# Kernel optimization log

Hardware: AMD Instinct MI355X
Metric: run time of the kernel (lower is better)

Reference implementation:

```python
import jax, jax.numpy as jnp
import numpy as np

S, B, C = 7, 2, 20          # YOLOv1 grid / boxes / classes
NE = B * 5 + C              # 30 channels per cell
BATCH = 32768
NBOX = 4                    # ground-truth boxes per image
L_COORD = 5.0


def _encode_np(boxes, classes):
    """Vectorized numpy replica of YoloLoss.encode, including its quirks:
    conf written at channel 4 + S*k (=> 4 and 11), class at channel 10 which is
    then overwritten by wh_y*S via the s+2:s+4 slice for k=1 (s=7 -> 9:11).
    boxes: [N, nb, 4] in xyxy, classes: [N, nb] int."""
    N, nb = classes.shape
    t = np.zeros((N, S, S, NE), np.float32)
    wh = boxes[:, :, 2:] - boxes[:, :, :2]
    cxcy = (boxes[:, :, 2:] + boxes[:, :, :2]) / 2.0
    cell = 1.0 / S
    ij = np.ceil(cxcy / cell) - 1.0                 # [N, nb, 2] (col, row)
    ijc = np.clip(ij, 0, S - 1).astype(np.int64)
    img = np.repeat(np.arange(N), nb)
    col = ijc[:, :, 0].ravel()
    row = ijc[:, :, 1].ravel()
    whf = (wh * S).reshape(-1, 2).astype(np.float32)
    delta = ((cxcy - ij * cell) / cell).reshape(-1, 2).astype(np.float32)
    cls = classes.ravel().astype(np.float32)
    t[img, row, col, 4] = 1.0          # conf, k=0 (4 + S*0)
    t[img, row, col, 11] = 1.0         # conf, k=1 (4 + S*1)
    t[img, row, col, 10] = cls         # class id (will be clobbered below)
    t[img, row, col, 2:4] = whf        # k=0 wh
    t[img, row, col, 0:2] = delta      # k=0 xy
    t[img, row, col, 9:11] = whf       # k=1 wh -- overwrites channel 10!
    t[img, row, col, 7:9] = delta      # k=1 xy
    return t.reshape(N, S * S, NE)


def setup_inputs() -> dict:
    key = jax.random.key(0)
    prediction = jax.random.normal(key, (BATCH, S * S, NE), dtype=jnp.float32)
    rng = np.random.default_rng(0)
    cxcy = rng.uniform(0.15, 0.85, (BATCH, NBOX, 2)).astype(np.float32)
    wh = rng.uniform(0.05, 0.3, (BATCH, NBOX, 2)).astype(np.float32)
    boxes = np.concatenate([cxcy - wh / 2, cxcy + wh / 2], axis=-1)  # xyxy
    classes = rng.integers(0, C, (BATCH, NBOX))
    target = jnp.asarray(_encode_np(boxes, classes))
    return {"prediction": prediction, "target": target}


def _point_form(b):
    # cxcywh -> xyxy on last axis
    return jnp.concatenate([b[..., :2] - b[..., 2:4] / 2,
                            b[..., :2] + b[..., 2:4] / 2], axis=-1)


def _iou(a, b):
    # a: [..., Bp, 4], b: [..., Bt, 4] (xyxy) -> [..., Bp, Bt]
    a = a[..., :, None, :]
    b = b[..., None, :, :]
    lo = jnp.maximum(a[..., :2], b[..., :2])
    hi = jnp.minimum(a[..., 2:], b[..., 2:])
    inter = jnp.prod(jnp.clip(hi - lo, 0.0, None), axis=-1)
    area_a = jnp.prod(a[..., 2:] - a[..., :2], axis=-1)
    area_b = jnp.prod(b[..., 2:] - b[..., :2], axis=-1)
    return inter / (area_a + area_b - inter + 1e-12)


def reference(prediction, target):
    coord = target[:, :, 4] > 0                         # [N, G] cells with objects
    bp = prediction[:, :, :B * 5].reshape(*prediction.shape[:2], B, 5)
    bt = target[:, :, :B * 5].reshape(*target.shape[:2], B, 5)

    # responsible-box matching: iou[bp_i, bt_j], argmax over predicted boxes per target box
    iou = _iou(_point_form(bp[..., :4]), _point_form(bt[..., :4]))  # [N,G,Bp,Bt]
    idx = jnp.argmax(iou, axis=-2)                                  # [N,G,Bt]
    resp = (jax.nn.one_hot(idx, B, dtype=jnp.float32).sum(-2) > 0)  # dedup, [N,G,B]
    resp = resp & coord[..., None]
    resp_f = resp.astype(jnp.float32)
    cnt = jnp.maximum(resp_f.sum(), 1.0)

    # containment loss: BCE-with-logits, mean over responsible boxes
    conf_p = bp[..., 4]
    conf_t = bt[..., 4]
    bce = jnp.logaddexp(0.0, conf_p) - conf_p * conf_t
    contain_loss = jnp.sum(bce * resp_f) / cnt

    # localization loss: mean MSE on xy + mean MSE on wh over responsible boxes
    sq_xy = (bp[..., 0:2] - bt[..., 0:2]) ** 2
    sq_wh = (bp[..., 2:4] - bt[..., 2:4]) ** 2
    loc_loss = (jnp.sum(sq_xy * resp_f[..., None]) / (2.0 * cnt)
                + jnp.sum(sq_wh * resp_f[..., None]) / (2.0 * cnt))

    # class loss: cross-entropy, mean over object cells
    logits = prediction[:, :, B * 5:]                               # [N,G,C]
    cls = jnp.clip(jnp.floor(target[:, :, B * 5]), 0, C - 1).astype(jnp.int32)
    lsm = jax.nn.log_softmax(logits, axis=-1)
    nll = -jnp.take_along_axis(lsm, cls[..., None], axis=-1)[..., 0]
    coord_f = coord.astype(jnp.float32)
    class_loss = jnp.sum(nll * coord_f) / jnp.maximum(coord_f.sum(), 1.0)

    # NOTE: original also computes l_noobj * noobj MSE into total_loss but then
    # returns class + contain + l_coord*loc, so noobj is dead code.
    return class_loss + contain_loss + L_COORD * loc_loss
```

## Files before the change

kernel.cpp:

```cpp
#include <hip/hip_runtime.h>
#include <math.h>

#define NCELL (32768 * 49)
#define NE 30
#define NC 20
#define G1 2048
#define BLK 256
#define TTOT (G1 * BLK)


__device__ __forceinline__ void process_cell(
    const float* __restrict__ pred, const float* __restrict__ targ, int cell,
    float& a0, float& a1, float& a2, float& a3, float& a4, float& a5) {

    const float2* p2 = reinterpret_cast<const float2*>(pred + (size_t)cell * NE);
    const float2* t2 = reinterpret_cast<const float2*>(targ + (size_t)cell * NE);

    float p[30], t[12];
    #pragma unroll
    for (int i = 0; i < 15; ++i) { float2 v = p2[i]; p[2*i] = v.x; p[2*i+1] = v.y; }
    #pragma unroll
    for (int i = 0; i < 6; ++i)  { float2 v = t2[i]; t[2*i] = v.x; t[2*i+1] = v.y; }

    float iou[2][2];
    #pragma unroll
    for (int i = 0; i < 2; ++i) {
        const float pcx = p[5*i], pcy = p[5*i+1], pw = p[5*i+2], ph = p[5*i+3];
        const float alx = pcx - pw*0.5f, aly = pcy - ph*0.5f;
        const float ahx = pcx + pw*0.5f, ahy = pcy + ph*0.5f;
        const float area_a = pw * ph;
        #pragma unroll
        for (int j = 0; j < 2; ++j) {
            const float tcx = t[5*j], tcy = t[5*j+1], tw = t[5*j+2], th = t[5*j+3];
            const float blx = tcx - tw*0.5f, bly = tcy - th*0.5f;
            const float bhx = tcx + tw*0.5f, bhy = tcy + th*0.5f;
            float ix = fminf(ahx, bhx) - fmaxf(alx, blx);
            float iy = fminf(ahy, bhy) - fmaxf(aly, bly);
            ix = fmaxf(ix, 0.f); iy = fmaxf(iy, 0.f);
            const float inter = ix * iy;
            const float area_b = tw * th;
            iou[i][j] = inter / (area_a + area_b - inter + 1e-12f);
        }
    }
    const int idx0 = (iou[1][0] > iou[0][0]) ? 1 : 0;
    const int idx1 = (iou[1][1] > iou[0][1]) ? 1 : 0;

    #pragma unroll
    for (int k = 0; k < 2; ++k) {
        const bool resp = (idx0 == k || idx1 == k);
        if (resp) {
            a0 += 1.f;
            const float cp = p[5*k+4], ct = t[5*k+4];
            a1 += fmaxf(cp, 0.f) + log1pf(expf(-fabsf(cp))) - cp * ct;
            const float dx = p[5*k]   - t[5*k];
            const float dy = p[5*k+1] - t[5*k+1];
            a2 += dx*dx + dy*dy;
            const float dw = p[5*k+2] - t[5*k+2];
            const float dh = p[5*k+3] - t[5*k+3];
            a3 += dw*dw + dh*dh;
        }
    }

    a5 += 1.f;
    const float cf = fminf(fmaxf(floorf(t[10]), 0.f), 19.f);
    const int cls = (int)cf;
    float m = p[10];
    #pragma unroll
    for (int c = 1; c < NC; ++c) m = fmaxf(m, p[10 + c]);
    float se = 0.f;
    float sel = 0.f;
    #pragma unroll
    for (int c = 0; c < NC; ++c) {
        se += expf(p[10 + c] - m);
        sel += (c == cls) ? p[10 + c] : 0.f;
    }
    a4 += -(sel - m - logf(se));
}

__global__ __launch_bounds__(BLK) void yolo_partial(
    const float* __restrict__ pred,
    const float* __restrict__ targ,
    float* __restrict__ partial) {

    float a0 = 0.f, a1 = 0.f, a2 = 0.f, a3 = 0.f, a4 = 0.f, a5 = 0.f;

    const int tid = blockIdx.x * BLK + threadIdx.x;

    float t4v[4];
    t4v[0] = targ[(size_t)(tid)            * NE + 4];
    t4v[1] = targ[(size_t)(tid + TTOT)     * NE + 4];
    t4v[2] = targ[(size_t)(tid + 2 * TTOT) * NE + 4];
    t4v[3] = (tid + 3 * TTOT < NCELL) ? targ[(size_t)(tid + 3 * TTOT) * NE + 4] : 0.f;

    if (t4v[0] > 0.f) process_cell(pred, targ, tid,            a0, a1, a2, a3, a4, a5);
    if (t4v[1] > 0.f) process_cell(pred, targ, tid + TTOT,     a0, a1, a2, a3, a4, a5);
    if (t4v[2] > 0.f) process_cell(pred, targ, tid + 2 * TTOT, a0, a1, a2, a3, a4, a5);
    if (t4v[3] > 0.f) process_cell(pred, targ, tid + 3 * TTOT, a0, a1, a2, a3, a4, a5);

    #pragma unroll
    for (int off = 32; off > 0; off >>= 1) {
        a0 += __shfl_down(a0, off, 64);
        a1 += __shfl_down(a1, off, 64);
        a2 += __shfl_down(a2, off, 64);
        a3 += __shfl_down(a3, off, 64);
        a4 += __shfl_down(a4, off, 64);
        a5 += __shfl_down(a5, off, 64);
    }

    __shared__ float sm[4][6];
    const int wave = threadIdx.x >> 6;
    const int lane = threadIdx.x & 63;
    if (lane == 0) {
        sm[wave][0] = a0; sm[wave][1] = a1; sm[wave][2] = a2;
        sm[wave][3] = a3; sm[wave][4] = a4; sm[wave][5] = a5;
    }
    __syncthreads();
    if (threadIdx.x == 0) {
        #pragma unroll
        for (int k = 0; k < 6; ++k) {
            float s = sm[0][k] + sm[1][k] + sm[2][k] + sm[3][k];
            partial[blockIdx.x * 6 + k] = s;
        }
    }
}

__global__ __launch_bounds__(BLK) void yolo_final(
    const float* __restrict__ partial, float* __restrict__ out) {
    __shared__ double sm[BLK][6];
    double a[6] = {0, 0, 0, 0, 0, 0};
    for (int i = threadIdx.x; i < G1; i += BLK) {
        #pragma unroll
        for (int k = 0; k < 6; ++k) a[k] += (double)partial[i * 6 + k];
    }
    #pragma unroll
    for (int k = 0; k < 6; ++k) sm[threadIdx.x][k] = a[k];
    __syncthreads();
    for (int off = BLK / 2; off > 0; off >>= 1) {
        if (threadIdx.x < off) {
            #pragma unroll
            for (int k = 0; k < 6; ++k) sm[threadIdx.x][k] += sm[threadIdx.x + off][k];
        }
        __syncthreads();
    }
    if (threadIdx.x == 0) {
        const double resp_sum  = sm[0][0];
        const double bce_sum   = sm[0][1];
        const double sqxy_sum  = sm[0][2];
        const double sqwh_sum  = sm[0][3];
        const double nll_sum   = sm[0][4];
        const double coord_sum = sm[0][5];
        const double cnt = fmax(resp_sum, 1.0);
        const double contain_loss = bce_sum / cnt;
        const double loc_loss = (sqxy_sum + sqwh_sum) / (2.0 * cnt);
        const double class_loss = nll_sum / fmax(coord_sum, 1.0);
        out[0] = (float)(class_loss + contain_loss + 5.0 * loc_loss);
    }
}

extern "C" void kernel_launch(void* const* d_in, const int* in_sizes, int n_in,
                              void* d_out, int out_size, void* d_ws, size_t ws_size,
                              hipStream_t stream) {
    const float* pred = (const float*)d_in[0];
    const float* targ = (const float*)d_in[1];
    float* partial = (float*)d_ws;

    yolo_partial<<<G1, BLK, 0, stream>>>(pred, targ, partial);
    yolo_final<<<1, BLK, 0, stream>>>(partial, (float*)d_out);
}
```

Baseline: 56.99 us.

## Compact object cells per block via ballot before processing

Each block now owns a contiguous chunk of 1024 cells. It scans their confidence flags, uses a wave ballot and prefix popcount to build a compacted list of object cells in shared memory, and then processes that list with all threads in the block. This replaces the old scheme, where each thread checked four cells spread across the grid and ran the heavy per-cell work under divergent branches. The aim is to avoid wasted SIMD lanes on the sparse object cells, at the cost of an extra barrier and shared-memory indexing.

Measured after the change: 49.03 us. -14.0%, faster.

```diff
diff --git a/kernel.cpp b/kernel.cpp
--- a/kernel.cpp
+++ b/kernel.cpp
@@ -4,9 +4,9 @@
 #define NCELL (32768 * 49)
 #define NE 30
 #define NC 20
-#define G1 2048
+#define G1 1568
 #define BLK 256
-#define TTOT (G1 * BLK)
+#define CPB 1024
 
 
 __device__ __forceinline__ void process_cell(
@@ -82,20 +82,43 @@
     const float* __restrict__ targ,
     float* __restrict__ partial) {
 
+    const int base = blockIdx.x * CPB;
+    const int tid  = threadIdx.x;
+    const int wave = tid >> 6;
+    const int lane = tid & 63;
+
+    float t4v[4];
+    #pragma unroll
+    for (int k = 0; k < 4; ++k)
+        t4v[k] = targ[(size_t)(base + k * BLK + tid) * NE + 4];
+
+    __shared__ int s_idx[4][256];
+    __shared__ int s_cnt[4];
+    int cnt = 0;
+    #pragma unroll
+    for (int k = 0; k < 4; ++k) {
+        const bool c = t4v[k] > 0.f;
+        const unsigned long long m = __ballot(c);
+        const int pre = __popcll(m & ((1ull << lane) - 1ull));
+        if (c) s_idx[wave][cnt + pre] = k * BLK + tid;
+        cnt += __popcll(m);
+    }
+    if (lane == 0) s_cnt[wave] = cnt;
+    __syncthreads();
+
+    const int c0 = s_cnt[0], c1 = s_cnt[1], c2 = s_cnt[2], c3 = s_cnt[3];
+    const int total = c0 + c1 + c2 + c3;
+
     float a0 = 0.f, a1 = 0.f, a2 = 0.f, a3 = 0.f, a4 = 0.f, a5 = 0.f;
 
-    const int tid = blockIdx.x * BLK + threadIdx.x;
-
-    float t4v[4];
-    t4v[0] = targ[(size_t)(tid)            * NE + 4];
-    t4v[1] = targ[(size_t)(tid + TTOT)     * NE + 4];
-    t4v[2] = targ[(size_t)(tid + 2 * TTOT) * NE + 4];
-    t4v[3] = (tid + 3 * TTOT < NCELL) ? targ[(size_t)(tid + 3 * TTOT) * NE + 4] : 0.f;
-
-    if (t4v[0] > 0.f) process_cell(pred, targ, tid,            a0, a1, a2, a3, a4, a5);
-    if (t4v[1] > 0.f) process_cell(pred, targ, tid + TTOT,     a0, a1, a2, a3, a4, a5);
-    if (t4v[2] > 0.f) process_cell(pred, targ, tid + 2 * TTOT, a0, a1, a2, a3, a4, a5);
-    if (t4v[3] > 0.f) process_cell(pred, targ, tid + 3 * TTOT, a0, a1, a2, a3, a4, a5);
+    for (int i = tid; i < total; i += BLK) {
+        int j = i, w = 0;
+        if (j >= c0) { j -= c0; w = 1;
+            if (j >= c1) { j -= c1; w = 2;
+                if (j >= c2) { j -= c2; w = 3; } } }
+        const int loc = s_idx[w][j];
+        process_cell(pred, targ, base + loc, a0, a1, a2, a3, a4, a5);
+    }
 
     #pragma unroll
     for (int off = 32; off > 0; off >>= 1) {
@@ -108,14 +131,12 @@
     }
 
     __shared__ float sm[4][6];
-    const int wave = threadIdx.x >> 6;
-    const int lane = threadIdx.x & 63;
     if (lane == 0) {
         sm[wave][0] = a0; sm[wave][1] = a1; sm[wave][2] = a2;
         sm[wave][3] = a3; sm[wave][4] = a4; sm[wave][5] = a5;
     }
     __syncthreads();
-    if (threadIdx.x == 0) {
+    if (tid == 0) {
         #pragma unroll
         for (int k = 0; k < 6; ++k) {
             float s = sm[0][k] + sm[1][k] + sm[2][k] + sm[3][k];
```
